# Performance work log

Hardware: AMD Instinct MI355X
Metric: run time of the kernel (lower is better)

The kernel has to match this reference:

```python
import jax, jax.numpy as jnp
import numpy as np

EMBED_DIM = 512
NUM_HEADS = 8
TGT_LEN = 1024
BSZ = 16


def setup_inputs() -> dict:
    key = jax.random.key(0)
    ks = jax.random.split(key, 6)
    E = EMBED_DIM
    query = jax.random.normal(ks[0], (TGT_LEN, BSZ, E), jnp.float32)
    i_proj = jax.random.normal(ks[1], (3 * E,), jnp.float32)
    # xavier_uniform-ish scale for (3E, E)
    lim = (6.0 / (3 * E + E)) ** 0.5
    in_proj_weight = jax.random.uniform(ks[2], (3 * E, E), jnp.float32, -lim, lim)
    in_proj_bias = jnp.zeros((3 * E,), jnp.float32)
    lim2 = (6.0 / (2 * E)) ** 0.5
    out_w = jax.random.uniform(ks[3], (E, E), jnp.float32, -lim2, lim2)
    out_b = jnp.zeros((E,), jnp.float32)
    bias_k = jax.random.normal(ks[4], (1, 1, E), jnp.float32)
    bias_v = jax.random.normal(ks[5], (1, 1, E), jnp.float32)
    return dict(query=query, i_proj=i_proj, in_proj_weight=in_proj_weight,
                in_proj_bias=in_proj_bias, out_w=out_w, out_b=out_b,
                bias_k=bias_k, bias_v=bias_v)


def reference(query, i_proj, in_proj_weight, in_proj_bias, out_w, out_b, bias_k, bias_v):
    # qkv_same path: key = value = query (self-attention)
    T, B, E = query.shape
    H = NUM_HEADS
    hd = E // H
    scaling = hd ** -0.5
    # per-call weight mutation: every 3rd column replaced by i_proj
    w = in_proj_weight.at[:, ::3].set(i_proj[:, None])
    qkv = jnp.einsum('tbe,fe->tbf', query, w) + in_proj_bias  # (T, B, 3E)
    q, k, v = jnp.split(qkv, 3, axis=-1)
    q = q * scaling
    k = jnp.concatenate([k, jnp.broadcast_to(bias_k, (1, B, E))], axis=0)  # (T+1, B, E)
    v = jnp.concatenate([v, jnp.broadcast_to(bias_v, (1, B, E))], axis=0)
    S = k.shape[0]
    q = q.reshape(T, B * H, hd).transpose(1, 0, 2)  # (B*H, T, hd)
    k = k.reshape(S, B * H, hd).transpose(1, 0, 2)  # (B*H, S, hd)
    v = v.reshape(S, B * H, hd).transpose(1, 0, 2)
    aw = jnp.einsum('nth,nsh->nts', q, k)  # (B*H, T, S)
    # global min-max normalization over the entire score tensor (not softmax)
    mn = jnp.min(aw)
    mx = jnp.max(aw)
    aw = (aw - mn) / (mx - mn)
    attn = jnp.einsum('nts,nsh->nth', aw, v)  # (B*H, T, hd)
    attn = attn.transpose(1, 0, 2).reshape(T, B, E)
    attn = attn @ out_w.T + out_b  # out_proj
    aw_avg = aw.reshape(B, H, T, S).sum(axis=1) / H  # (B, T, S)
    wq, wk, wv = jnp.split(w, 3, axis=0)
    w_ret = jnp.stack([wq.T, wk.T, wv.T], axis=0)  # (3, E, E)
    return attn, aw_avg, w_ret
```

## Files before the change

### kernel.cpp

```cpp
#include <hip/hip_runtime.h>
#include <hip/hip_bf16.h>
#include <stdint.h>

typedef __bf16 bf16;
typedef __bf16 bf16x8 __attribute__((ext_vector_type(8)));
typedef __bf16 bf16x4 __attribute__((ext_vector_type(4)));
typedef float  f32x4  __attribute__((ext_vector_type(4)));

#define MFMA_BF16(a,b,c) __builtin_amdgcn_mfma_f32_16x16x32_bf16((a),(b),(c),0,0,0)

#define WS_QBF_IN  0L
#define WS_WBF     16777216L
#define WS_OUTWBF  18350080L
#define WS_Q       18874368L
#define WS_K       35651584L
#define WS_V       52428800L
#define WS_VT      69206016L
#define WS_AWLAST  85983232L
#define WS_VCS     86507520L
#define WS_MM      86540288L
#define WS_KT      86540544L
#define WS_KTV     103317760L

__device__ __forceinline__ void gload16(const void* g, void* l) {
  __builtin_amdgcn_global_load_lds((const __attribute__((address_space(1))) uint32_t*)g,
                                   (__attribute__((address_space(3))) uint32_t*)l, 16, 0, 0);
}
__device__ __forceinline__ unsigned ordf(float x) {
  unsigned b = __float_as_uint(x);
  return (b & 0x80000000u) ? ~b : (b | 0x80000000u);
}
__device__ __forceinline__ float deordf(unsigned u) {
  unsigned b = (u & 0x80000000u) ? (u ^ 0x80000000u) : ~u;
  return __uint_as_float(b);
}

__global__ __launch_bounds__(256) void cvt_query_kernel(const float* __restrict__ in,
                                                        bf16* __restrict__ out) {
  long i = (long)blockIdx.x * 256 + threadIdx.x;
  for (; i < 2097152L; i += (long)gridDim.x * 256) {
    float4 v = ((const float4*)in)[i];
    bf16x4 o; o[0] = (bf16)v.x; o[1] = (bf16)v.y; o[2] = (bf16)v.z; o[3] = (bf16)v.w;
    ((bf16x4*)out)[i] = o;
  }
}

__global__ __launch_bounds__(256) void prep_weights_kernel(
    const float* __restrict__ in_w, const float* __restrict__ i_proj,
    const float* __restrict__ out_w, bf16* __restrict__ w_bf,
    bf16* __restrict__ outw_bf, float* __restrict__ w_ret,
    unsigned* __restrict__ mm) {
  long idx = (long)blockIdx.x * 256 + threadIdx.x;
  if (idx == 0) { mm[0] = 0xFFFFFFFFu; mm[1] = 0u; }
  if (idx < 786432L) {
    int f = (int)(idx >> 9), e = (int)(idx & 511);
    float val = (e % 3 == 0) ? i_proj[f] : in_w[idx];
    w_bf[idx] = (bf16)val;
    w_ret[(long)(f >> 9) * 262144 + (long)e * 512 + (f & 511)] = val;
  } else if (idx < 1048576L) {
    long j = idx - 786432L;
    outw_bf[j] = (bf16)out_w[j];
  }
}

template <int MODE>
__global__ __launch_bounds__(256, 2) void gemm_kernel(
    const bf16* __restrict__ A, const bf16* __restrict__ B,
    const float* __restrict__ bias,
    bf16* __restrict__ q_out, bf16* __restrict__ k_out, bf16* __restrict__ v_out,
    float* __restrict__ outC) {
  const int K = 512;
  __shared__ __align__(16) bf16 aTile[128 * 32];
  __shared__ __align__(16) bf16 bTile[128 * 32];
  const int tid = threadIdx.x;
  const int lane = tid & 63, w = tid >> 6;
  const int l15 = lane & 15, l4 = lane >> 4;
  const long r0 = (long)blockIdx.y * 128;
  const long f0 = (long)blockIdx.x * 128;
  const int rm = (w >> 1) * 64, cn = (w & 1) * 64;
  const int srow = tid >> 2;
  const int scc = tid & 3;
  f32x4 acc[4][4] = {};

  for (int kk = 0; kk < K; kk += 32) {
#pragma unroll
    for (int i = 0; i < 2; ++i) {
      int row = srow + i * 64;
      int cc = scc ^ (row & 3);
      gload16(A + (r0 + row) * K + kk + cc * 8, (char*)aTile + (w * 64 + i * 256) * 16);
    }
#pragma unroll
    for (int i = 0; i < 2; ++i) {
      int row = srow + i * 64;
      int cc = scc ^ (row & 3);
      gload16(B + (f0 + row) * K + kk + cc * 8, (char*)bTile + (w * 64 + i * 256) * 16);
    }
    __syncthreads();
    bf16x8 af[4], bfr[4];
#pragma unroll
    for (int mi = 0; mi < 4; ++mi) {
      int r = rm + mi * 16 + l15;
      int c = l4 ^ (r & 3);
      af[mi] = *(const bf16x8*)((const char*)aTile + r * 64 + c * 16);
    }
#pragma unroll
    for (int ni = 0; ni < 4; ++ni) {
      int r = cn + ni * 16 + l15;
      int c = l4 ^ (r & 3);
      bfr[ni] = *(const bf16x8*)((const char*)bTile + r * 64 + c * 16);
    }
#pragma unroll
    for (int mi = 0; mi < 4; ++mi)
#pragma unroll
      for (int ni = 0; ni < 4; ++ni)
        acc[mi][ni] = MFMA_BF16(af[mi], bfr[ni], acc[mi][ni]);
    __syncthreads();
  }
#pragma unroll
  for (int mi = 0; mi < 4; ++mi)
#pragma unroll
    for (int ni = 0; ni < 4; ++ni)
#pragma unroll
      for (int r = 0; r < 4; ++r) {
        long row = r0 + rm + mi * 16 + l4 * 4 + r;
        int f = (int)f0 + cn + ni * 16 + l15;
        float val = acc[mi][ni][r] + bias[f];
        if (MODE == 0) {
          int t = (int)(row >> 4), b = (int)(row & 15);
          int which = f >> 9, hh = (f >> 6) & 7, d = f & 63;
          long off = ((long)(b * 8 + hh) * 1024 + t) * 64 + d;
          if (which == 0)      q_out[off] = (bf16)(val * 0.125f);
          else if (which == 1) k_out[off] = (bf16)val;
          else                 v_out[off] = (bf16)val;
        } else {
          outC[row * 512 + f] = val;
        }
      }
}

#define AWS_STAGE(kk, buf)                                                            \
  do {                                                                                \
    int h_ = (kk) >> 1, db_ = ((kk) & 1) * 32;                                        \
    _Pragma("unroll")                                                                 \
    for (int i_ = 0; i_ < 2; ++i_) {                                                  \
      int row_ = srow + i_ * 64;                                                      \
      int cc_ = scc ^ (row_ & 3);                                                     \
      gload16(q_bf + ((long)(b * 8 + h_) * 1024 + t0 + row_) * 64 + db_ + cc_ * 8,    \
              (char*)aT[buf] + (w * 64 + i_ * 256) * 16);                             \
      gload16(k_bf + ((long)(b * 8 + h_) * 1024 + s0 + row_) * 64 + db_ + cc_ * 8,    \
              (char*)bT[buf] + (w * 64 + i_ * 256) * 16);                             \
    }                                                                                 \
  } while (0)

#define AWS_COMPUTE(buf)                                                              \
  do {                                                                                \
    bf16x8 af[4], bfr[4];                                                             \
    _Pragma("unroll")                                                                 \
    for (int mi_ = 0; mi_ < 4; ++mi_) {                                               \
      int r_ = rm + mi_ * 16 + l15;                                                   \
      int c_ = l4 ^ (r_ & 3);                                                         \
      af[mi_] = *(const bf16x8*)((const char*)aT[buf] + r_ * 64 + c_ * 16);           \
    }                                                                                 \
    _Pragma("unroll")                                                                 \
    for (int ni_ = 0; ni_ < 4; ++ni_) {                                               \
      int r_ = cn + ni_ * 16 + l15;                                                   \
      int c_ = l4 ^ (r_ & 3);                                                         \
      bfr[ni_] = *(const bf16x8*)((const char*)bT[buf] + r_ * 64 + c_ * 16);          \
    }                                                                                 \
    _Pragma("unroll")                                                                 \
    for (int mi_ = 0; mi_ < 4; ++mi_)                                                 \
      _Pragma("unroll")                                                               \
      for (int ni_ = 0; ni_ < 4; ++ni_)                                               \
        acc[mi_][ni_] = MFMA_BF16(af[mi_], bfr[ni_], acc[mi_][ni_]);                  \
  } while (0)

__global__ __launch_bounds__(256, 2) void awsum_gemm_kernel(
    const bf16* __restrict__ q_bf, const bf16* __restrict__ k_bf,
    bf16* __restrict__ aw_raw, unsigned* __restrict__ mm) {
  __shared__ __align__(16) bf16 aT[2][128 * 32];
  __shared__ __align__(16) bf16 bT[2][128 * 32];
  const int tid = threadIdx.x;
  const int lane = tid & 63, w = tid >> 6;
  const int l15 = lane & 15, l4 = lane >> 4;
  const int bid = blockIdx.x;
  const int xcd = bid & 7, slot = bid >> 3;
  const int b = xcd * 2 + (slot >> 6);
  const int rest = slot & 63;
  const int t0 = (rest >> 3) * 128;
  const int s0 = (rest & 7) * 128;
  const int rm = (w >> 1) * 64, cn = (w & 1) * 64;
  const int srow = tid >> 2;
  const int scc = tid & 3;

  f32x4 acc[4][4] = {};
  f32x4 snap[4][4] = {};
  float vmin = 1e30f, vmax = -1e30f;

  AWS_STAGE(0, 0);
  __syncthreads();
  for (int h = 0; h < 8; ++h) {
    AWS_STAGE(2 * h + 1, 1);
    AWS_COMPUTE(0);
    __syncthreads();
    if (h < 7) AWS_STAGE(2 * h + 2, 0);
    AWS_COMPUTE(1);
#pragma unroll
    for (int mi = 0; mi < 4; ++mi)
#pragma unroll
      for (int ni = 0; ni < 4; ++ni) {
        f32x4 d = acc[mi][ni] - snap[mi][ni];
#pragma unroll
        for (int r = 0; r < 4; ++r) {
          vmin = fminf(vmin, d[r]);
          vmax = fmaxf(vmax, d[r]);
        }
        snap[mi][ni] = acc[mi][ni];
      }
    __syncthreads();
  }
#pragma unroll
  for (int mi = 0; mi < 4; ++mi)
#pragma unroll
    for (int ni = 0; ni < 4; ++ni)
#pragma unroll
      for (int r = 0; r < 4; ++r) {
        int t = t0 + rm + mi * 16 + l4 * 4 + r;
        int s = s0 + cn + ni * 16 + l15;
        aw_raw[((long)b * 1024 + t) * 1024 + s] = (bf16)acc[mi][ni][r];
      }
#pragma unroll
  for (int off = 32; off; off >>= 1) {
    vmin = fminf(vmin, __shfl_xor(vmin, off));
    vmax = fmaxf(vmax, __shfl_xor(vmax, off));
  }
  if (lane == 0) { atomicMin(&mm[0], ordf(vmin)); atomicMax(&mm[1], ordf(vmax)); }
}

__global__ __launch_bounds__(256) void transpose_kv_kernel(
    const bf16* __restrict__ k_bf, const bf16* __restrict__ v_bf,
    bf16* __restrict__ kT, bf16* __restrict__ vT) {
  const bf16* src = blockIdx.z ? v_bf : k_bf;
  bf16* dst = blockIdx.z ? vT : kT;
  const int n = blockIdx.y;
  const long s0 = (long)blockIdx.x * 64;
  __shared__ __align__(16) bf16 tile[64][72];
  const int tid = threadIdx.x;
  const int row = tid >> 3, cc = tid & 7;
#pragma unroll
  for (int it = 0; it < 2; ++it) {
    int r = row + it * 32;
    bf16x8 vv = *(const bf16x8*)(src + ((long)n * 1024 + s0 + r) * 64 + cc * 8);
    *(bf16x8*)&tile[r][cc * 8] = vv;
  }
  __syncthreads();
#pragma unroll
  for (int it = 0; it < 2; ++it) {
    int d = row + it * 32;
    bf16x8 ov;
#pragma unroll
    for (int j = 0; j < 8; ++j) ov[j] = tile[cc * 8 + j][d];
    *(bf16x8*)(dst + ((long)n * 64 + d) * 1024 + s0 + cc * 8) = ov;
  }
}

__global__ __launch_bounds__(256) void vcolsum_kernel(const bf16* __restrict__ vT,
                                                      const float* __restrict__ bias_v,
                                                      float* __restrict__ vcs) {
  const int n = blockIdx.x, h = n & 7;
  const int d = threadIdx.x >> 2, q = threadIdx.x & 3;
  float acc = 0.f;
  const bf16* row = vT + (long)n * 65536 + (long)d * 1024 + q * 256;
#pragma unroll 4
  for (int j = 0; j < 32; ++j) {
    bf16x8 v = *(const bf16x8*)(row + j * 8);
#pragma unroll
    for (int e = 0; e < 8; ++e) acc += (float)v[e];
  }
  __shared__ float red[256];
  red[threadIdx.x] = acc;
  __syncthreads();
  if (q == 0)
    vcs[n * 64 + d] = red[d * 4] + red[d * 4 + 1] + red[d * 4 + 2] + red[d * 4 + 3] +
                      bias_v[h * 64 + d];
}

__global__ __launch_bounds__(256) void ktv_kernel(const bf16* __restrict__ kT,
                                                  const bf16* __restrict__ vT,
                                                  bf16* __restrict__ ktvT) {
  const int n = blockIdx.x;
  const int tid = threadIdx.x;
  const int lane = tid & 63, w = tid >> 6;
  const int l15 = lane & 15, l4 = lane >> 4;
  const int wr = w >> 1, wc = w & 1;
  f32x4 acc[2][2] = {};
  const bf16* kbase = kT + (long)n * 65536;
  const bf16* vbase = vT + (long)n * 65536;
  for (int s0 = 0; s0 < 1024; s0 += 32) {
    bf16x8 af[2], bfr[2];
#pragma unroll
    for (int mi = 0; mi < 2; ++mi)
      af[mi] = *(const bf16x8*)(kbase + (long)(wr * 32 + mi * 16 + l15) * 1024 + s0 + l4 * 8);
#pragma unroll
    for (int ni = 0; ni < 2; ++ni)
      bfr[ni] = *(const bf16x8*)(vbase + (long)(wc * 32 + ni * 16 + l15) * 1024 + s0 + l4 * 8);
#pragma unroll
    for (int mi = 0; mi < 2; ++mi)
#pragma unroll
      for (int ni = 0; ni < 2; ++ni)
        acc[mi][ni] = MFMA_BF16(af[mi], bfr[ni], acc[mi][ni]);
  }
#pragma unroll
  for (int mi = 0; mi < 2; ++mi)
#pragma unroll
    for (int ni = 0; ni < 2; ++ni)
#pragma unroll
      for (int r = 0; r < 4; ++r) {
        int d = wr * 32 + mi * 16 + l4 * 4 + r;
        int dp = wc * 32 + ni * 16 + l15;
        ktvT[(long)n * 4096 + dp * 64 + d] = (bf16)acc[mi][ni][r];
      }
}

__global__ __launch_bounds__(256) void qattn_kernel(
    const bf16* __restrict__ q_bf, const bf16* __restrict__ ktvT,
    const float* __restrict__ aw_last, const float* __restrict__ vcs,
    const float* __restrict__ bias_v, const unsigned* __restrict__ mm,
    bf16* __restrict__ A2) {
  const int tid = threadIdx.x;
  const int lane = tid & 63, w = tid >> 6;
  const int l15 = lane & 15, l4 = lane >> 4;
  const int t0 = blockIdx.x * 64;
  const int h = blockIdx.y * 4 + w;
  const int b = blockIdx.z;
  const long n = (long)b * 8 + h;
  f32x4 acc[4][4] = {};
  const bf16* qbase = q_bf + (n * 1024 + t0) * 64;
  const bf16* kbase = ktvT + (long)n * 4096;
#pragma unroll
  for (int kk = 0; kk < 64; kk += 32) {
    bf16x8 af[4], bfr[4];
#pragma unroll
    for (int mi = 0; mi < 4; ++mi)
      af[mi] = *(const bf16x8*)(qbase + (mi * 16 + l15) * 64 + kk + l4 * 8);
#pragma unroll
    for (int ni = 0; ni < 4; ++ni)
      bfr[ni] = *(const bf16x8*)(kbase + (ni * 16 + l15) * 64 + kk + l4 * 8);
#pragma unroll
    for (int mi = 0; mi < 4; ++mi)
#pragma unroll
      for (int ni = 0; ni < 4; ++ni)
        acc[mi][ni] = MFMA_BF16(af[mi], bfr[ni], acc[mi][ni]);
  }
  float mn = deordf(mm[0]), mx = deordf(mm[1]);
  float a = 1.f / (mx - mn), c = -mn * a;
#pragma unroll
  for (int mi = 0; mi < 4; ++mi)
#pragma unroll
    for (int r = 0; r < 4; ++r) {
      int t = t0 + mi * 16 + l4 * 4 + r;
      float alast = a * aw_last[n * 1024 + t];
#pragma unroll
      for (int ni = 0; ni < 4; ++ni) {
        int dp = ni * 16 + l15;
        float val = a * acc[mi][ni][r] + alast * bias_v[h * 64 + dp] + c * vcs[n * 64 + dp];
        A2[((long)t * 16 + b) * 512 + h * 64 + dp] = (bf16)val;
      }
    }
}

__global__ __launch_bounds__(256) void bias_col_kernel(const bf16* __restrict__ q_bf,
                                                       const float* __restrict__ bias_k,
                                                       float* __restrict__ aw_last,
                                                       unsigned* __restrict__ mm) {
  const int n = blockIdx.y, h = n & 7;
  const int t = blockIdx.x * 256 + threadIdx.x;
  float acc = 0.f;
  const bf16* qrow = q_bf + ((long)n * 1024 + t) * 64;
#pragma unroll
  for (int j = 0; j < 8; ++j) {
    bf16x8 qv = *(const bf16x8*)(qrow + j * 8);
#pragma unroll
    for (int e = 0; e < 8; ++e) acc += (float)qv[e] * bias_k[h * 64 + j * 8 + e];
  }
  aw_last[(long)n * 1024 + t] = acc;
  float vmin = acc, vmax = acc;
#pragma unroll
  for (int off = 32; off; off >>= 1) {
    vmin = fminf(vmin, __shfl_xor(vmin, off));
    vmax = fmaxf(vmax, __shfl_xor(vmax, off));
  }
  if ((threadIdx.x & 63) == 0) { atomicMin(&mm[0], ordf(vmin)); atomicMax(&mm[1], ordf(vmax)); }
}

__global__ __launch_bounds__(256) void rescale_kernel(const bf16* __restrict__ aw_raw,
                                                      float* __restrict__ aw_out,
                                                      const float* __restrict__ aw_last,
                                                      const unsigned* __restrict__ mm) {
  long idx = (long)blockIdx.x * 256 + threadIdx.x;
  float mn = deordf(mm[0]), mx = deordf(mm[1]);
  float a = 1.f / (mx - mn), c = -mn * a;
  int s = (int)(idx % 1025);
  long bt = idx / 1025;
  float v;
  if (s < 1024) {
    v = (float)aw_raw[bt * 1024 + s];
  } else {
    int b = (int)(bt >> 10), t = (int)(bt & 1023);
    v = 0.f;
#pragma unroll
    for (int h = 0; h < 8; ++h) v += aw_last[(long)(b * 8 + h) * 1024 + t];
  }
  aw_out[idx] = fmaf(a, v * 0.125f, c);
}

extern "C" void kernel_launch(void* const* d_in, const int* in_sizes, int n_in,
                              void* d_out, int out_size, void* d_ws, size_t ws_size,
                              hipStream_t stream) {
  const float* query  = (const float*)d_in[0];
  const float* i_proj = (const float*)d_in[1];
  const float* in_w   = (const float*)d_in[2];
  const float* in_b   = (const float*)d_in[3];
  const float* out_w  = (const float*)d_in[4];
  const float* out_b  = (const float*)d_in[5];
  const float* bias_k = (const float*)d_in[6];
  const float* bias_v = (const float*)d_in[7];
  float* out = (float*)d_out;

  char* ws = (char*)d_ws;
  bf16* qbf_in = (bf16*)(ws + WS_QBF_IN);
  bf16* w_bf   = (bf16*)(ws + WS_WBF);
  bf16* outwbf = (bf16*)(ws + WS_OUTWBF);
  bf16* q_bf   = (bf16*)(ws + WS_Q);
  bf16* k_bf   = (bf16*)(ws + WS_K);
  bf16* v_bf   = (bf16*)(ws + WS_V);
  bf16* vT     = (bf16*)(ws + WS_VT);
  bf16* kT     = (bf16*)(ws + WS_KT);
  bf16* ktvT   = (bf16*)(ws + WS_KTV);
  bf16* aw_raw = (bf16*)(ws + WS_V);
  float* aw_last = (float*)(ws + WS_AWLAST);
  float* vcs     = (float*)(ws + WS_VCS);
  unsigned* mm   = (unsigned*)(ws + WS_MM);
  bf16* A2 = qbf_in;

  float* out_attn  = out;
  float* out_awavg = out + 8388608L;
  float* out_wret  = out + 25182208L;

  cvt_query_kernel<<<2048, 256, 0, stream>>>(query, qbf_in);
  prep_weights_kernel<<<4096, 256, 0, stream>>>(in_w, i_proj, out_w, w_bf, outwbf, out_wret, mm);
  gemm_kernel<0><<<dim3(12, 128), 256, 0, stream>>>(qbf_in, w_bf, in_b, q_bf, k_bf, v_bf, nullptr);
  transpose_kv_kernel<<<dim3(16, 128, 2), 256, 0, stream>>>(k_bf, v_bf, kT, vT);
  vcolsum_kernel<<<128, 256, 0, stream>>>(vT, bias_v, vcs);
  bias_col_kernel<<<dim3(4, 128), 256, 0, stream>>>(q_bf, bias_k, aw_last, mm);
  ktv_kernel<<<128, 256, 0, stream>>>(kT, vT, ktvT);
  awsum_gemm_kernel<<<1024, 256, 0, stream>>>(q_bf, k_bf, aw_raw, mm);
  rescale_kernel<<<65600, 256, 0, stream>>>(aw_raw, out_awavg, aw_last, mm);
  qattn_kernel<<<dim3(16, 2, 16), 256, 0, stream>>>(q_bf, ktvT, aw_last, vcs, bias_v, mm, A2);
  gemm_kernel<1><<<dim3(4, 128), 256, 0, stream>>>(A2, outwbf, out_b, nullptr, nullptr, nullptr, out_attn);
}
```

Measured before the change: 318.2 us.

## Stage full head (K=64) per LDS buffer with prefetch-two pipeline in awsum GEMM

The awsum score GEMM now loads an entire 64-wide head slice per LDS stage instead of two 32-wide halves. It keeps two heads in flight using explicit vmcnt waits and raw s_barrier with sched_barrier, replacing __syncthreads. The XOR swizzle widens to 8 chunks to suit the 128-byte rows. This halves the number of sync points and lets global loads overlap compute more deeply, at the cost of doubling LDS use per block, which may affect 2-block occupancy.

```diff
diff --git a/kernel.cpp b/kernel.cpp
--- a/kernel.cpp
+++ b/kernel.cpp
@@ -138,47 +138,48 @@
       }
 }
 
-#define AWS_STAGE(kk, buf)                                                            \
-  do {                                                                                \
-    int h_ = (kk) >> 1, db_ = ((kk) & 1) * 32;                                        \
-    _Pragma("unroll")                                                                 \
-    for (int i_ = 0; i_ < 2; ++i_) {                                                  \
-      int row_ = srow + i_ * 64;                                                      \
-      int cc_ = scc ^ (row_ & 3);                                                     \
-      gload16(q_bf + ((long)(b * 8 + h_) * 1024 + t0 + row_) * 64 + db_ + cc_ * 8,    \
-              (char*)aT[buf] + (w * 64 + i_ * 256) * 16);                             \
-      gload16(k_bf + ((long)(b * 8 + h_) * 1024 + s0 + row_) * 64 + db_ + cc_ * 8,    \
-              (char*)bT[buf] + (w * 64 + i_ * 256) * 16);                             \
-    }                                                                                 \
+#define AWS_STAGE(h_, buf_)                                                        \
+  do {                                                                             \
+    _Pragma("unroll")                                                              \
+    for (int i_ = 0; i_ < 4; ++i_) {                                               \
+      int row_ = i_ * 32 + wrow;                                                   \
+      gload16(q_bf + ((long)(b * 8 + (h_)) * 1024 + t0 + row_) * 64 + scc8 * 8,    \
+              (char*)aT[buf_] + (i_ * 256 + w * 64) * 16);                         \
+      gload16(k_bf + ((long)(b * 8 + (h_)) * 1024 + s0 + row_) * 64 + scc8 * 8,    \
+              (char*)bT[buf_] + (i_ * 256 + w * 64) * 16);                         \
+    }                                                                              \
   } while (0)
 
-#define AWS_COMPUTE(buf)                                                              \
-  do {                                                                                \
-    bf16x8 af[4], bfr[4];                                                             \
-    _Pragma("unroll")                                                                 \
-    for (int mi_ = 0; mi_ < 4; ++mi_) {                                               \
-      int r_ = rm + mi_ * 16 + l15;                                                   \
-      int c_ = l4 ^ (r_ & 3);                                                         \
-      af[mi_] = *(const bf16x8*)((const char*)aT[buf] + r_ * 64 + c_ * 16);           \
-    }                                                                                 \
-    _Pragma("unroll")                                                                 \
-    for (int ni_ = 0; ni_ < 4; ++ni_) {                                               \
-      int r_ = cn + ni_ * 16 + l15;                                                   \
-      int c_ = l4 ^ (r_ & 3);                                                         \
-      bfr[ni_] = *(const bf16x8*)((const char*)bT[buf] + r_ * 64 + c_ * 16);          \
-    }                                                                                 \
-    _Pragma("unroll")                                                                 \
-    for (int mi_ = 0; mi_ < 4; ++mi_)                                                 \
-      _Pragma("unroll")                                                               \
-      for (int ni_ = 0; ni_ < 4; ++ni_)                                               \
-        acc[mi_][ni_] = MFMA_BF16(af[mi_], bfr[ni_], acc[mi_][ni_]);                  \
+#define AWS_COMPUTE(buf_)                                                          \
+  do {                                                                             \
+    _Pragma("unroll")                                                              \
+    for (int ks_ = 0; ks_ < 2; ++ks_) {                                            \
+      bf16x8 af[4], bfr[4];                                                        \
+      _Pragma("unroll")                                                            \
+      for (int mi_ = 0; mi_ < 4; ++mi_) {                                          \
+        int r_ = rm + mi_ * 16 + l15;                                              \
+        int p_ = (ks_ * 4 + l4) ^ (r_ & 7);                                        \
+        af[mi_] = *(const bf16x8*)((const char*)aT[buf_] + r_ * 128 + p_ * 16);    \
+      }                                                                            \
+      _Pragma("unroll")                                                            \
+      for (int ni_ = 0; ni_ < 4; ++ni_) {                                          \
+        int r_ = cn + ni_ * 16 + l15;                                              \
+        int p_ = (ks_ * 4 + l4) ^ (r_ & 7);                                        \
+        bfr[ni_] = *(const bf16x8*)((const char*)bT[buf_] + r_ * 128 + p_ * 16);   \
+      }                                                                            \
+      _Pragma("unroll")                                                            \
+      for (int mi_ = 0; mi_ < 4; ++mi_)                                            \
+        _Pragma("unroll")                                                          \
+        for (int ni_ = 0; ni_ < 4; ++ni_)                                          \
+          acc[mi_][ni_] = MFMA_BF16(af[mi_], bfr[ni_], acc[mi_][ni_]);             \
+    }                                                                              \
   } while (0)
 
 __global__ __launch_bounds__(256, 2) void awsum_gemm_kernel(
     const bf16* __restrict__ q_bf, const bf16* __restrict__ k_bf,
     bf16* __restrict__ aw_raw, unsigned* __restrict__ mm) {
-  __shared__ __align__(16) bf16 aT[2][128 * 32];
-  __shared__ __align__(16) bf16 bT[2][128 * 32];
+  __shared__ __align__(16) bf16 aT[2][128 * 64];
+  __shared__ __align__(16) bf16 bT[2][128 * 64];
   const int tid = threadIdx.x;
   const int lane = tid & 63, w = tid >> 6;
   const int l15 = lane & 15, l4 = lane >> 4;
@@ -189,21 +190,21 @@
   const int t0 = (rest >> 3) * 128;
   const int s0 = (rest & 7) * 128;
   const int rm = (w >> 1) * 64, cn = (w & 1) * 64;
-  const int srow = tid >> 2;
-  const int scc = tid & 3;
+  const int wrow = w * 8 + (lane >> 3);
+  const int scc8 = (lane & 7) ^ ((lane >> 3) & 7);
 
   f32x4 acc[4][4] = {};
   f32x4 snap[4][4] = {};
   float vmin = 1e30f, vmax = -1e30f;
 
   AWS_STAGE(0, 0);
-  __syncthreads();
+  AWS_STAGE(1, 1);
+  asm volatile("s_waitcnt vmcnt(8)" ::: "memory");
+  __builtin_amdgcn_s_barrier();
+  __builtin_amdgcn_sched_barrier(0);
+#pragma unroll
   for (int h = 0; h < 8; ++h) {
-    AWS_STAGE(2 * h + 1, 1);
-    AWS_COMPUTE(0);
-    __syncthreads();
-    if (h < 7) AWS_STAGE(2 * h + 2, 0);
-    AWS_COMPUTE(1);
+    AWS_COMPUTE(h & 1);
 #pragma unroll
     for (int mi = 0; mi < 4; ++mi)
 #pragma unroll
@@ -216,7 +217,15 @@
         }
         snap[mi][ni] = acc[mi][ni];
       }
-    __syncthreads();
+    __builtin_amdgcn_s_barrier();
+    __builtin_amdgcn_sched_barrier(0);
+    if (h + 2 < 8) AWS_STAGE(h + 2, h & 1);
+    if (h + 1 < 8) {
+      if (h + 2 < 8) asm volatile("s_waitcnt vmcnt(8)" ::: "memory");
+      else           asm volatile("s_waitcnt vmcnt(0)" ::: "memory");
+      __builtin_amdgcn_s_barrier();
+      __builtin_amdgcn_sched_barrier(0);
+    }
   }
 #pragma unroll
   for (int mi = 0; mi < 4; ++mi)
```

Result: faster. 311.8 us (-2.0%).
